# Kernel optimization log

Hardware: AMD Instinct MI355X
Metric: run time of the kernel (lower is better)

The kernel has to match this reference:

```python
import jax, jax.numpy as jnp
import numpy as np

B, C, CI, H, W = 8, 1024, 512, 56, 56
BN_EPS = 1e-5


def setup_inputs() -> dict:
    key = jax.random.key(0)
    ks = jax.random.split(key, 12)
    s_in = 1.0 / np.sqrt(C)
    s_mid = 1.0 / np.sqrt(CI)
    return {
        "x1": jax.random.normal(ks[0], (B, C, H, W), jnp.float32),
        "x2": jax.random.normal(ks[1], (B, C, H, W), jnp.float32),
        "g_w": jax.random.normal(ks[2], (CI, C), jnp.float32) * s_in,
        "g_b": jax.random.normal(ks[3], (CI,), jnp.float32) * s_in,
        "theta_w": jax.random.normal(ks[4], (CI, C), jnp.float32) * s_in,
        "theta_b": jax.random.normal(ks[5], (CI,), jnp.float32) * s_in,
        "phi_w": jax.random.normal(ks[6], (CI, C), jnp.float32) * s_in,
        "phi_b": jax.random.normal(ks[7], (CI,), jnp.float32) * s_in,
        "wz_w": jax.random.normal(ks[8], (C, CI), jnp.float32) * s_mid,
        "wz_b": jax.random.normal(ks[9], (C,), jnp.float32) * s_mid,
        "bn_gamma": jax.random.normal(ks[10], (C,), jnp.float32) * 0.1 + 1.0,
        "bn_beta": jax.random.normal(ks[11], (C,), jnp.float32) * 0.1,
    }


def reference(x1, x2, g_w, g_b, theta_w, theta_b, phi_w, phi_b, wz_w, wz_b, bn_gamma, bn_beta):
    b, c, h, w = x1.shape
    n = h * w
    # flatten spatial, channels-last: (B, N, C); 1x1 conv == per-position matmul
    x1f = x1.reshape(b, c, n).transpose(0, 2, 1)
    x2f = x2.reshape(b, c, n).transpose(0, 2, 1)
    g_x = x2f @ g_w.T + g_b            # (B, N, CI)
    th = x1f @ theta_w.T + theta_b     # (B, N, CI)
    ph = x2f @ phi_w.T + phi_b         # (B, N, CI)
    f = jnp.einsum("bnd,bmd->bnm", th, ph)   # (B, N, N) affinity
    attn = jax.nn.softmax(f, axis=-1)         # embedded-gaussian
    y = jnp.einsum("bnm,bmd->bnd", attn, g_x)  # (B, N, CI)
    wy = y @ wz_w.T + wz_b             # (B, N, C)
    # BatchNorm (training mode: batch statistics over batch+spatial dims)
    mu = wy.mean(axis=(0, 1))
    var = wy.var(axis=(0, 1))
    wy = (wy - mu) * jax.lax.rsqrt(var + BN_EPS) * bn_gamma + bn_beta
    z = wy + x1f                       # residual
    return z.transpose(0, 2, 1).reshape(b, c, h, w)
```

## Files before the change

### kernel.cpp

```cpp
#include <hip/hip_runtime.h>


typedef _Float16 half8 __attribute__((ext_vector_type(8)));
typedef float floatx4 __attribute__((ext_vector_type(4)));

constexpr int B_ = 8, C_ = 1024, CI_ = 512, N_ = 3136;
constexpr int M_ = B_ * N_;
constexpr float BN_EPS = 1e-5f;

constexpr size_t XT1_OFF = 0;
constexpr size_t XT2_OFF = XT1_OFF + (size_t)M_ * C_ * 2;
constexpr size_t WTH_OFF = XT2_OFF + (size_t)M_ * C_ * 2;
constexpr size_t WPH_OFF = WTH_OFF + (size_t)CI_ * C_ * 2;
constexpr size_t WG_OFF  = WPH_OFF + (size_t)CI_ * C_ * 2;
constexpr size_t WZB_OFF = WG_OFF  + (size_t)CI_ * C_ * 2;
constexpr size_t TH_OFF  = WZB_OFF + (size_t)C_ * CI_ * 2;
constexpr size_t PH_OFF  = TH_OFF  + (size_t)M_ * CI_ * 2;
constexpr size_t GXT_OFF = PH_OFF  + (size_t)M_ * CI_ * 2;
constexpr size_t Y_OFF   = GXT_OFF + (size_t)M_ * CI_ * 2;
constexpr size_t WY_OFF  = Y_OFF   + (size_t)M_ * CI_ * 2;
constexpr size_t SSUM_OFF= WY_OFF  + (size_t)M_ * C_ * 2;
constexpr size_t SSQ_OFF = SSUM_OFF + 4096;
constexpr size_t SC_OFF  = SSQ_OFF + 4096;

__device__ __forceinline__ ushort f2h(float f) {
    _Float16 h = (_Float16)f;
    union { _Float16 h; ushort u; } v; v.h = h;
    return v.u;
}
__device__ __forceinline__ float h2f(ushort u) {
    union { ushort u; _Float16 h; } v; v.u = u;
    return (float)v.h;
}

__global__ __launch_bounds__(256) void cvtw4(const float* __restrict__ a, const float* __restrict__ b,
                                             const float* __restrict__ c, const float* __restrict__ d,
                                             ushort* oa, ushort* ob, ushort* oc, ushort* od) {
    const float* s; ushort* o;
    switch (blockIdx.y) {
        case 0: s = a; o = oa; break;
        case 1: s = b; o = ob; break;
        case 2: s = c; o = oc; break;
        default: s = d; o = od; break;
    }
    int i = (blockIdx.x * 256 + threadIdx.x) * 4;
    float4 v = *(const float4*)&s[i];
    ushort4 u; u.x = f2h(v.x); u.y = f2h(v.y); u.z = f2h(v.z); u.w = f2h(v.w);
    *(ushort4*)&o[i] = u;
}

__global__ __launch_bounds__(256) void xpose(const float* __restrict__ x, ushort* __restrict__ xt) {
    __shared__ ushort T[64 * 68];
    const int b = blockIdx.z, n0 = blockIdx.y * 64, c0 = blockIdx.x * 64;
    const int t = threadIdx.x;
    {
        const int cl = t >> 4, jb = (t & 15) * 4;
        #pragma unroll
        for (int i = 0; i < 4; ++i) {
            int c = cl + i * 16;
            float4 v = *(const float4*)&x[((size_t)b * C_ + c0 + c) * N_ + n0 + jb];
            ushort4 u; u.x = f2h(v.x); u.y = f2h(v.y); u.z = f2h(v.z); u.w = f2h(v.w);
            *(ushort4*)&T[c * 68 + jb] = u;
        }
    }
    __syncthreads();
    {
        const int nl = t >> 4, cb = (t & 15) * 4;
        #pragma unroll
        for (int i = 0; i < 4; ++i) {
            int n = nl + i * 16;
            ushort4 u;
            u.x = T[(cb + 0) * 68 + n];
            u.y = T[(cb + 1) * 68 + n];
            u.z = T[(cb + 2) * 68 + n];
            u.w = T[(cb + 3) * 68 + n];
            *(ushort4*)&xt[((size_t)b * N_ + n0 + n) * C_ + c0 + cb] = u;
        }
    }
}

template<int K, int NOUT, int MODE>
__global__ __launch_bounds__(256, 2) void gemm_bt(
    const ushort* __restrict__ A, const ushort* __restrict__ Bt,
    const float* __restrict__ bias, ushort* __restrict__ outb,
    float* __restrict__ ssum, float* __restrict__ ssq)
{
    __shared__ ushort Als[128 * 40];
    __shared__ ushort Bls[128 * 40];
    const int t = threadIdx.x;
    const int w = t >> 6, l = t & 63, quad = l >> 4, lid = l & 15;
    const int rw = w & 1, cw = w >> 1;
    const int rowbase = blockIdx.y * 128, colbase = blockIdx.x * 128;

    floatx4 acc[4][4] = {};

    for (int ks = 0; ks < K / 32; ++ks) {
        __syncthreads();
        #pragma unroll
        for (int i = 0; i < 2; ++i) {
            int idx = t + i * 256;
            int row = idx >> 2, ch = idx & 3;
            *(uint4*)&Als[row * 40 + ch * 8] =
                *(const uint4*)&A[(size_t)(rowbase + row) * K + ks * 32 + ch * 8];
            *(uint4*)&Bls[row * 40 + ch * 8] =
                *(const uint4*)&Bt[(size_t)(colbase + row) * K + ks * 32 + ch * 8];
        }
        __syncthreads();
        half8 af[4];
        #pragma unroll
        for (int rt = 0; rt < 4; ++rt)
            af[rt] = *(const half8*)&Als[(rw * 64 + rt * 16 + lid) * 40 + quad * 8];
        #pragma unroll
        for (int ct = 0; ct < 4; ++ct) {
            half8 bf = *(const half8*)&Bls[(cw * 64 + ct * 16 + lid) * 40 + quad * 8];
            #pragma unroll
            for (int rt = 0; rt < 4; ++rt)
                acc[rt][ct] = __builtin_amdgcn_mfma_f32_16x16x32_f16(af[rt], bf, acc[rt][ct], 0, 0, 0);
        }
    }

    #pragma unroll
    for (int ct = 0; ct < 4; ++ct) {
        const int col = colbase + cw * 64 + ct * 16 + lid;
        const float bv = bias[col];
        float s = 0.f, q = 0.f;
        #pragma unroll
        for (int rt = 0; rt < 4; ++rt) {
            const int row0 = rowbase + rw * 64 + rt * 16 + quad * 4;
            if constexpr (MODE == 1) {
                const int bb = row0 / N_;
                const int nn = row0 - bb * N_;
                ushort4 u;
                u.x = f2h(acc[rt][ct][0] + bv);
                u.y = f2h(acc[rt][ct][1] + bv);
                u.z = f2h(acc[rt][ct][2] + bv);
                u.w = f2h(acc[rt][ct][3] + bv);
                *(ushort4*)&outb[((size_t)bb * CI_ + col) * N_ + nn] = u;
            } else {
                #pragma unroll
                for (int r = 0; r < 4; ++r) {
                    float v = acc[rt][ct][r] + bv;
                    outb[(size_t)(row0 + r) * NOUT + col] = f2h(v);
                    if constexpr (MODE == 2) { s += v; q += v * v; }
                }
            }
        }
        if constexpr (MODE == 2) {
            s += __shfl_xor(s, 16, 64); s += __shfl_xor(s, 32, 64);
            q += __shfl_xor(q, 16, 64); q += __shfl_xor(q, 32, 64);
            if (quad == 0) {
                atomicAdd(&ssum[col], s);
                atomicAdd(&ssq[col], q);
            }
        }
    }
}

__global__ __launch_bounds__(512, 2) void attn(
    const ushort* __restrict__ TH, const ushort* __restrict__ PH,
    const ushort* __restrict__ GXT, ushort* __restrict__ Y)
{
    __shared__ ushort STR[20480];
    __shared__ float  Ss[64 * 33];
    __shared__ ushort Ps[64 * 40];
    __shared__ float  mrow[64], lrow[64], arow[64];
    __shared__ float  red[64 * 8];

    const int t = threadIdx.x;
    const int w = t >> 6, l = t & 63, quad = l >> 4, lid = l & 15;
    const int rw = w & 3;
    const int dh = w >> 2;
    const int b = blockIdx.x / 49, q = blockIdx.x % 49;
    const int n0 = q * 64;
    const int srow = t >> 3, sj = t & 7;

    half8 thr[16];
    {
        const size_t baseTH = ((size_t)b * N_ + n0 + rw * 16 + lid) * CI_;
        #pragma unroll
        for (int kc = 0; kc < 16; ++kc)
            thr[kc] = *(const half8*)&TH[baseTH + kc * 32 + quad * 8];
    }
    if (t < 64) { mrow[t] = -1e30f; lrow[t] = 0.f; }
    floatx4 acc[16] = {};

    for (int s = 0; s < N_ / 32; ++s) {
        const int m0 = s * 32;
        __syncthreads();
        {
            const size_t basePH = ((size_t)b * N_ + m0) * CI_;
            #pragma unroll
            for (int i = 0; i < 4; ++i) {
                int idx = t + i * 512;
                int row = idx >> 6, ch = idx & 63;
                *(uint4*)&STR[row * 520 + ch * 8] =
                    *(const uint4*)&PH[basePH + (size_t)row * CI_ + ch * 8];
            }
        }
        __syncthreads();
        {
            floatx4 sacc = {};
            #pragma unroll
            for (int ks = 0; ks < 16; ++ks) {
                half8 bb = *(const half8*)&STR[(dh * 16 + lid) * 520 + ks * 32 + quad * 8];
                sacc = __builtin_amdgcn_mfma_f32_16x16x32_f16(thr[ks], bb, sacc, 0, 0, 0);
            }
            const int col = dh * 16 + lid;
            #pragma unroll
            for (int r = 0; r < 4; ++r)
                Ss[(rw * 16 + quad * 4 + r) * 33 + col] = sacc[r];
        }
        __syncthreads();
        {
            const size_t baseGX = (size_t)b * CI_ * N_ + m0;
            #pragma unroll
            for (int i = 0; i < 4; ++i) {
                int idx = t + i * 512;
                int d = idx >> 2, ch = idx & 3;
                *(uint4*)&STR[d * 40 + ch * 8] =
                    *(const uint4*)&GXT[baseGX + (size_t)d * N_ + ch * 8];
            }
        }
        {
            float pm = Ss[srow * 33 + sj * 4];
            pm = fmaxf(pm, Ss[srow * 33 + sj * 4 + 1]);
            pm = fmaxf(pm, Ss[srow * 33 + sj * 4 + 2]);
            pm = fmaxf(pm, Ss[srow * 33 + sj * 4 + 3]);
            red[srow * 8 + sj] = pm;
        }
        __syncthreads();
        if (sj == 0) {
            float m_ = red[srow * 8];
            #pragma unroll
            for (int k = 1; k < 8; ++k) m_ = fmaxf(m_, red[srow * 8 + k]);
            const float mo = mrow[srow];
            const float mn = fmaxf(mo, m_);
            mrow[srow] = mn;
            arow[srow] = __expf(mo - mn);
        }
        __syncthreads();
        {
            const float mn = mrow[srow];
            float ps = 0.f;
            #pragma unroll
            for (int k = 0; k < 4; ++k) {
                float p = __expf(Ss[srow * 33 + sj * 4 + k] - mn);
                Ps[srow * 40 + sj * 4 + k] = f2h(p);
                ps += p;
            }
            red[srow * 8 + sj] = ps;
        }
        {
            float al[4];
            #pragma unroll
            for (int r = 0; r < 4; ++r) al[r] = arow[rw * 16 + quad * 4 + r];
            #pragma unroll
            for (int ctl = 0; ctl < 16; ++ctl)
                #pragma unroll
                for (int r = 0; r < 4; ++r) acc[ctl][r] *= al[r];
        }
        __syncthreads();
        if (sj == 0) {
            float sm = 0.f;
            #pragma unroll
            for (int k = 0; k < 8; ++k) sm += red[srow * 8 + k];
            lrow[srow] = lrow[srow] * arow[srow] + sm;
        }
        {
            half8 a = *(const half8*)&Ps[(rw * 16 + lid) * 40 + quad * 8];
            #pragma unroll
            for (int ctl = 0; ctl < 16; ++ctl) {
                half8 bb = *(const half8*)&STR[(dh * 256 + ctl * 16 + lid) * 40 + quad * 8];
                acc[ctl] = __builtin_amdgcn_mfma_f32_16x16x32_f16(a, bb, acc[ctl], 0, 0, 0);
            }
        }
    }
    __syncthreads();
    float inv[4];
    #pragma unroll
    for (int r = 0; r < 4; ++r) inv[r] = 1.0f / lrow[rw * 16 + quad * 4 + r];
    const size_t baseY = ((size_t)b * N_ + n0) * CI_;
    #pragma unroll
    for (int ctl = 0; ctl < 16; ++ctl) {
        const int col = dh * 256 + ctl * 16 + lid;
        #pragma unroll
        for (int r = 0; r < 4; ++r) {
            const int row = rw * 16 + quad * 4 + r;
            Y[baseY + (size_t)row * CI_ + col] = f2h(acc[ctl][r] * inv[r]);
        }
    }
}

__global__ __launch_bounds__(256) void bnfin(const float* __restrict__ ssum, const float* __restrict__ ssq,
                                             const float* __restrict__ gamma, const float* __restrict__ beta,
                                             float* __restrict__ sc) {
    const int c = blockIdx.x * 256 + threadIdx.x;
    const float inv_m = 1.0f / (float)M_;
    const float mu = ssum[c] * inv_m;
    const float var = ssq[c] * inv_m - mu * mu;
    const float s = gamma[c] * rsqrtf(var + BN_EPS);
    sc[c] = s;
    sc[C_ + c] = beta[c] - mu * s;
}

__global__ __launch_bounds__(256) void fin(const ushort* __restrict__ wy, const float* __restrict__ x1,
                                           const float* __restrict__ sc, float* __restrict__ out) {
    __shared__ float T[64 * 65];
    const int b = blockIdx.z, n0 = blockIdx.y * 64, c0 = blockIdx.x * 64;
    const int t = threadIdx.x;
    {
        const int nl = t >> 4, cb = (t & 15) * 4;
        #pragma unroll
        for (int i = 0; i < 4; ++i) {
            int n = nl + i * 16;
            ushort4 u = *(const ushort4*)&wy[((size_t)b * N_ + n0 + n) * C_ + c0 + cb];
            T[(cb + 0) * 65 + n] = h2f(u.x);
            T[(cb + 1) * 65 + n] = h2f(u.y);
            T[(cb + 2) * 65 + n] = h2f(u.z);
            T[(cb + 3) * 65 + n] = h2f(u.w);
        }
    }
    __syncthreads();
    {
        const int cl = t >> 4, nb = (t & 15) * 4;
        #pragma unroll
        for (int i = 0; i < 4; ++i) {
            int c = cl + i * 16;
            const float scale = sc[c0 + c], shift = sc[C_ + c0 + c];
            float4 xv = *(const float4*)&x1[((size_t)b * C_ + c0 + c) * N_ + n0 + nb];
            float4 o;
            o.x = T[c * 65 + nb + 0] * scale + shift + xv.x;
            o.y = T[c * 65 + nb + 1] * scale + shift + xv.y;
            o.z = T[c * 65 + nb + 2] * scale + shift + xv.z;
            o.w = T[c * 65 + nb + 3] * scale + shift + xv.w;
            *(float4*)&out[((size_t)b * C_ + c0 + c) * N_ + n0 + nb] = o;
        }
    }
}

extern "C" void kernel_launch(void* const* d_in, const int* in_sizes, int n_in,
                              void* d_out, int out_size, void* d_ws, size_t ws_size,
                              hipStream_t stream) {
    const float* x1      = (const float*)d_in[0];
    const float* x2      = (const float*)d_in[1];
    const float* g_w     = (const float*)d_in[2];
    const float* g_b     = (const float*)d_in[3];
    const float* theta_w = (const float*)d_in[4];
    const float* theta_b = (const float*)d_in[5];
    const float* phi_w   = (const float*)d_in[6];
    const float* phi_b   = (const float*)d_in[7];
    const float* wz_w    = (const float*)d_in[8];
    const float* wz_b    = (const float*)d_in[9];
    const float* bn_g    = (const float*)d_in[10];
    const float* bn_b    = (const float*)d_in[11];
    float* out = (float*)d_out;

    char* ws = (char*)d_ws;
    ushort* XT1 = (ushort*)(ws + XT1_OFF);
    ushort* XT2 = (ushort*)(ws + XT2_OFF);
    ushort* WTH = (ushort*)(ws + WTH_OFF);
    ushort* WPH = (ushort*)(ws + WPH_OFF);
    ushort* WG  = (ushort*)(ws + WG_OFF);
    ushort* WZB = (ushort*)(ws + WZB_OFF);
    ushort* THp = (ushort*)(ws + TH_OFF);
    ushort* PHp = (ushort*)(ws + PH_OFF);
    ushort* GXTp= (ushort*)(ws + GXT_OFF);
    ushort* Yp  = (ushort*)(ws + Y_OFF);
    ushort* WYp = (ushort*)(ws + WY_OFF);
    float* ssum = (float*)(ws + SSUM_OFF);
    float* ssq  = (float*)(ws + SSQ_OFF);
    float* sc   = (float*)(ws + SC_OFF);

    hipMemsetAsync(ws + SSUM_OFF, 0, 8192, stream);

    cvtw4<<<dim3(512, 4), 256, 0, stream>>>(theta_w, phi_w, g_w, wz_w, WTH, WPH, WG, WZB);
    xpose<<<dim3(16, 49, 8), 256, 0, stream>>>(x1, XT1);
    xpose<<<dim3(16, 49, 8), 256, 0, stream>>>(x2, XT2);

    gemm_bt<1024, 512, 0><<<dim3(4, 196), 256, 0, stream>>>(XT1, WTH, theta_b, THp, nullptr, nullptr);
    gemm_bt<1024, 512, 0><<<dim3(4, 196), 256, 0, stream>>>(XT2, WPH, phi_b, PHp, nullptr, nullptr);
    gemm_bt<1024, 512, 1><<<dim3(4, 196), 256, 0, stream>>>(XT2, WG, g_b, GXTp, nullptr, nullptr);

    attn<<<dim3(B_ * 49), 512, 0, stream>>>(THp, PHp, GXTp, Yp);

    gemm_bt<512, 1024, 2><<<dim3(8, 196), 256, 0, stream>>>(Yp, WZB, wz_b, WYp, ssum, ssq);
    bnfin<<<dim3(4), 256, 0, stream>>>(ssum, ssq, bn_g, bn_b, sc);
    fin<<<dim3(16, 49, 8), 256, 0, stream>>>(WYp, x1, sc, out);
}
```

Baseline: 1.067 ms.

## Software-pipeline attention loop with register prefetch and fewer barriers

Restructures the flash-attention inner loop so the next tile's PH and GX loads are fetched into registers while the current tile is computed, then written into separate shared buffers for PH and GX. The softmax row max and sum are now done with wave shuffles instead of shared-memory reductions, which cuts the barriers per iteration from six to three. It also switches to exp2 with the log2(e) factor folded into the scores, skips rescaling the accumulator when no row max changed, and raises wave priority around the MFMA blocks. The prefetch raises register pressure and the barrier ordering needs care to stay race-free.

```diff
diff --git a/kernel.cpp b/kernel.cpp
--- a/kernel.cpp
+++ b/kernel.cpp
@@ -31,6 +31,11 @@
 __device__ __forceinline__ float h2f(ushort u) {
     union { ushort u; _Float16 h; } v; v.u = u;
     return (float)v.h;
+}
+
+__device__ __forceinline__ void bar_lgkm() {
+    asm volatile("s_waitcnt lgkmcnt(0)" ::: "memory");
+    __builtin_amdgcn_s_barrier();
 }
 
 __global__ __launch_bounds__(256) void cvtw4(const float* __restrict__ a, const float* __restrict__ b,
@@ -160,11 +165,11 @@
     const ushort* __restrict__ TH, const ushort* __restrict__ PH,
     const ushort* __restrict__ GXT, ushort* __restrict__ Y)
 {
-    __shared__ ushort STR[20480];
-    __shared__ float  Ss[64 * 33];
-    __shared__ ushort Ps[64 * 40];
-    __shared__ float  mrow[64], lrow[64], arow[64];
-    __shared__ float  red[64 * 8];
+    __shared__ __align__(16) ushort PHb[32 * 520];
+    __shared__ __align__(16) ushort GXb[512 * 40];
+    __shared__ __align__(16) float  Ss[64 * 36];
+    __shared__ __align__(16) ushort Ps[64 * 40];
+    __shared__ float mrow[64], lrow[64], arow[64];
 
     const int t = threadIdx.x;
     const int w = t >> 6, l = t & 63, quad = l >> 4, lid = l & 15;
@@ -174,6 +179,9 @@
     const int n0 = q * 64;
     const int srow = t >> 3, sj = t & 7;
 
+    const size_t basePH_b = (size_t)b * N_ * CI_;
+    const size_t baseGX_b = (size_t)b * CI_ * N_;
+
     half8 thr[16];
     {
         const size_t baseTH = ((size_t)b * N_ + n0 + rw * 16 + lid) * CI_;
@@ -181,101 +189,125 @@
         for (int kc = 0; kc < 16; ++kc)
             thr[kc] = *(const half8*)&TH[baseTH + kc * 32 + quad * 8];
     }
-    if (t < 64) { mrow[t] = -1e30f; lrow[t] = 0.f; }
+    if (t < 64) { mrow[t] = -1e30f; lrow[t] = 0.f; arow[t] = 1.f; }
+
+    uint4 phr[4], gxr[4];
+    #pragma unroll
+    for (int i = 0; i < 4; ++i) {
+        int idx = t + i * 512;
+        phr[i] = *(const uint4*)&PH[basePH_b + (size_t)(idx >> 6) * CI_ + (idx & 63) * 8];
+    }
+    #pragma unroll
+    for (int i = 0; i < 4; ++i) {
+        int idx = t + i * 512;
+        gxr[i] = *(const uint4*)&GXT[baseGX_b + (size_t)(idx >> 2) * N_ + (idx & 3) * 8];
+    }
+    #pragma unroll
+    for (int i = 0; i < 4; ++i) {
+        int idx = t + i * 512;
+        *(uint4*)&PHb[(idx >> 6) * 520 + (idx & 63) * 8] = phr[i];
+    }
+    bar_lgkm();
+
     floatx4 acc[16] = {};
 
-    for (int s = 0; s < N_ / 32; ++s) {
-        const int m0 = s * 32;
-        __syncthreads();
-        {
-            const size_t basePH = ((size_t)b * N_ + m0) * CI_;
+    for (int s = 0; s < 98; ++s) {
+        const int m0n = (s + 1) * 32;
+
+        if (s < 97) {
             #pragma unroll
             for (int i = 0; i < 4; ++i) {
                 int idx = t + i * 512;
-                int row = idx >> 6, ch = idx & 63;
-                *(uint4*)&STR[row * 520 + ch * 8] =
-                    *(const uint4*)&PH[basePH + (size_t)row * CI_ + ch * 8];
-            }
-        }
-        __syncthreads();
+                phr[i] = *(const uint4*)&PH[basePH_b + (size_t)(m0n + (idx >> 6)) * CI_ + (idx & 63) * 8];
+            }
+        }
         {
             floatx4 sacc = {};
+            __builtin_amdgcn_s_setprio(1);
             #pragma unroll
             for (int ks = 0; ks < 16; ++ks) {
-                half8 bb = *(const half8*)&STR[(dh * 16 + lid) * 520 + ks * 32 + quad * 8];
+                half8 bb = *(const half8*)&PHb[(dh * 16 + lid) * 520 + ks * 32 + quad * 8];
                 sacc = __builtin_amdgcn_mfma_f32_16x16x32_f16(thr[ks], bb, sacc, 0, 0, 0);
             }
+            __builtin_amdgcn_s_setprio(0);
             const int col = dh * 16 + lid;
             #pragma unroll
             for (int r = 0; r < 4; ++r)
-                Ss[(rw * 16 + quad * 4 + r) * 33 + col] = sacc[r];
-        }
-        __syncthreads();
-        {
-            const size_t baseGX = (size_t)b * CI_ * N_ + m0;
+                Ss[(rw * 16 + quad * 4 + r) * 36 + col] = sacc[r] * 1.44269504f;
+        }
+        #pragma unroll
+        for (int i = 0; i < 4; ++i) {
+            int idx = t + i * 512;
+            *(uint4*)&GXb[(idx >> 2) * 40 + (idx & 3) * 8] = gxr[i];
+        }
+        bar_lgkm();
+
+        if (s < 97) {
             #pragma unroll
             for (int i = 0; i < 4; ++i) {
                 int idx = t + i * 512;
-                int d = idx >> 2, ch = idx & 3;
-                *(uint4*)&STR[d * 40 + ch * 8] =
-                    *(const uint4*)&GXT[baseGX + (size_t)d * N_ + ch * 8];
+                gxr[i] = *(const uint4*)&GXT[baseGX_b + (size_t)(idx >> 2) * N_ + m0n + (idx & 3) * 8];
             }
         }
         {
-            float pm = Ss[srow * 33 + sj * 4];
-            pm = fmaxf(pm, Ss[srow * 33 + sj * 4 + 1]);
-            pm = fmaxf(pm, Ss[srow * 33 + sj * 4 + 2]);
-            pm = fmaxf(pm, Ss[srow * 33 + sj * 4 + 3]);
-            red[srow * 8 + sj] = pm;
-        }
-        __syncthreads();
-        if (sj == 0) {
-            float m_ = red[srow * 8];
-            #pragma unroll
-            for (int k = 1; k < 8; ++k) m_ = fmaxf(m_, red[srow * 8 + k]);
+            float4 s4 = *(const float4*)&Ss[srow * 36 + sj * 4];
+            float pm = fmaxf(fmaxf(s4.x, s4.y), fmaxf(s4.z, s4.w));
+            pm = fmaxf(pm, __shfl_xor(pm, 1));
+            pm = fmaxf(pm, __shfl_xor(pm, 2));
+            pm = fmaxf(pm, __shfl_xor(pm, 4));
             const float mo = mrow[srow];
-            const float mn = fmaxf(mo, m_);
-            mrow[srow] = mn;
-            arow[srow] = __expf(mo - mn);
-        }
-        __syncthreads();
+            const float mn = fmaxf(mo, pm);
+            const float al = exp2f(mo - mn);
+            const float p0 = exp2f(s4.x - mn);
+            const float p1 = exp2f(s4.y - mn);
+            const float p2 = exp2f(s4.z - mn);
+            const float p3 = exp2f(s4.w - mn);
+            ushort4 u; u.x = f2h(p0); u.y = f2h(p1); u.z = f2h(p2); u.w = f2h(p3);
+            *(ushort4*)&Ps[srow * 40 + sj * 4] = u;
+            float ps = p0 + p1 + p2 + p3;
+            ps += __shfl_xor(ps, 1);
+            ps += __shfl_xor(ps, 2);
+            ps += __shfl_xor(ps, 4);
+            if (sj == 0) {
+                mrow[srow] = mn;
+                arow[srow] = al;
+                lrow[srow] = lrow[srow] * al + ps;
+            }
+        }
+        bar_lgkm();
+
         {
-            const float mn = mrow[srow];
-            float ps = 0.f;
-            #pragma unroll
-            for (int k = 0; k < 4; ++k) {
-                float p = __expf(Ss[srow * 33 + sj * 4 + k] - mn);
-                Ps[srow * 40 + sj * 4 + k] = f2h(p);
-                ps += p;
-            }
-            red[srow * 8 + sj] = ps;
-        }
-        {
-            float al[4];
-            #pragma unroll
-            for (int r = 0; r < 4; ++r) al[r] = arow[rw * 16 + quad * 4 + r];
-            #pragma unroll
-            for (int ctl = 0; ctl < 16; ++ctl)
+            float al4[4];
+            #pragma unroll
+            for (int r = 0; r < 4; ++r) al4[r] = arow[rw * 16 + quad * 4 + r];
+            const bool need = (al4[0] != 1.f) | (al4[1] != 1.f) | (al4[2] != 1.f) | (al4[3] != 1.f);
+            if (__any(need)) {
                 #pragma unroll
-                for (int r = 0; r < 4; ++r) acc[ctl][r] *= al[r];
-        }
-        __syncthreads();
-        if (sj == 0) {
-            float sm = 0.f;
-            #pragma unroll
-            for (int k = 0; k < 8; ++k) sm += red[srow * 8 + k];
-            lrow[srow] = lrow[srow] * arow[srow] + sm;
+                for (int ctl = 0; ctl < 16; ++ctl)
+                    #pragma unroll
+                    for (int r = 0; r < 4; ++r) acc[ctl][r] *= al4[r];
+            }
         }
         {
             half8 a = *(const half8*)&Ps[(rw * 16 + lid) * 40 + quad * 8];
+            __builtin_amdgcn_s_setprio(1);
             #pragma unroll
             for (int ctl = 0; ctl < 16; ++ctl) {
-                half8 bb = *(const half8*)&STR[(dh * 256 + ctl * 16 + lid) * 40 + quad * 8];
+                half8 bb = *(const half8*)&GXb[(dh * 256 + ctl * 16 + lid) * 40 + quad * 8];
                 acc[ctl] = __builtin_amdgcn_mfma_f32_16x16x32_f16(a, bb, acc[ctl], 0, 0, 0);
             }
-        }
-    }
-    __syncthreads();
+            __builtin_amdgcn_s_setprio(0);
+        }
+        if (s < 97) {
+            #pragma unroll
+            for (int i = 0; i < 4; ++i) {
+                int idx = t + i * 512;
+                *(uint4*)&PHb[(idx >> 6) * 520 + (idx & 63) * 8] = phr[i];
+            }
+        }
+        bar_lgkm();
+    }
+
     float inv[4];
     #pragma unroll
     for (int r = 0; r < 4; ++r) inv[r] = 1.0f / lrow[rw * 16 + quad * 4 + r];
```

Result: slower. 1.144 ms (+7.2%).
